# Performance work log

Hardware: AMD Instinct MI355X
Metric: run time of the kernel (lower is better)

The kernel has to match this reference:

```python
import jax, jax.numpy as jnp
import numpy as np


def setup_inputs() -> dict:
    key = jax.random.key(0)
    ks = jax.random.split(key, 7)
    B, Q, K, H, D, R = 2, 2048, 2048, 16, 64, 32
    queries = jax.random.normal(ks[0], (B, Q, H, D), dtype=jnp.float32)
    keys = jax.random.normal(ks[1], (B, K, H, D), dtype=jnp.float32)
    values = jax.random.normal(ks[2], (B, K, H, D), dtype=jnp.float32)
    att_mask = jax.random.randint(ks[3], (B, Q, K), 0, 2, dtype=jnp.int32)
    relative_att_ids = jax.random.randint(ks[4], (B, Q, K), 0, R, dtype=jnp.int32)
    # TruncatedNormal(stddev=0.5) approximated by clipped normal
    relative_emb_table = jnp.clip(
        0.5 * jax.random.normal(ks[5], (R, H, D), dtype=jnp.float32), -1.0, 1.0)
    relative_bias_table = jnp.zeros((R, H), dtype=jnp.float32)
    return {
        'queries': queries,
        'keys': keys,
        'values': values,
        'att_mask': att_mask,
        'relative_att_ids': relative_att_ids,
        'relative_emb_table': relative_emb_table,
        'relative_bias_table': relative_bias_table,
    }


def reference(queries, keys, values, att_mask, relative_att_ids,
              relative_emb_table, relative_bias_table):
    # content scores: [B,Q,K,H]
    content = jnp.einsum('bqhd,bkhd->bqkh', queries, keys)
    # relative scores per vocab id: [B,Q,R,H]
    all_rel = jnp.einsum('bqhd,rhd->bqrh', queries, relative_emb_table)
    all_rel = all_rel + relative_bias_table  # broadcast [R,H]
    # gather along vocab axis per (q,k): [B,Q,K,H]
    rel = jnp.take_along_axis(
        all_rel, relative_att_ids[:, :, :, None].astype(jnp.int32), axis=2)
    scores = content + rel
    d = queries.shape[-1]
    scores = scores / jnp.sqrt(jnp.asarray(d, scores.dtype))
    mask_adder = -10000.0 * (1.0 - att_mask[:, :, :, None].astype(scores.dtype))
    scores = scores + mask_adder
    probs = jax.nn.softmax(scores, axis=-2)  # softmax over key axis
    return jnp.einsum('bqkh,bkhd->bqhd', probs, values)
```

## Files before the change

kernel.cpp:

```cpp
#include <hip/hip_runtime.h>
#include <hip/hip_fp16.h>
#include <stdint.h>

#define Bn 2
#define Qn 2048
#define Kn 2048
#define Hn 16
#define Dn 64
#define Rn 32

#define LOG2E_8 0.18033688011112042f
#define MASK_NEG -14426.950408889634f

typedef __attribute__((ext_vector_type(8))) short short8v;
typedef __attribute__((ext_vector_type(4))) float f32x4;
typedef __attribute__((ext_vector_type(4))) uint32_t u32x4;

static __device__ __forceinline__ uint16_t bf16rn(float f) {
  uint32_t u = __builtin_bit_cast(uint32_t, f);
  u += 0x7FFFu + ((u >> 16) & 1u);
  return (uint16_t)(u >> 16);
}
static __device__ __forceinline__ float bf16f(uint16_t h) {
  uint32_t u = ((uint32_t)h) << 16;
  return __builtin_bit_cast(float, u);
}
static __device__ __forceinline__ float exp2a(float x) {
  float r; asm("v_exp_f32 %0, %1" : "=v"(r) : "v"(x)); return r;
}
static __device__ __forceinline__ uint32_t cvtpk(float lo, float hi) {
  uint32_t r; asm("v_cvt_pk_bf16_f32 %0, %1, %2" : "=v"(r) : "v"(lo), "v"(hi)); return r;
}
static __device__ __forceinline__ void gl_lds16(const void* g, void* l) {
  __builtin_amdgcn_global_load_lds((const __attribute__((address_space(1))) void*)g,
                                   (__attribute__((address_space(3))) void*)l, 16, 0, 0);
}

__global__ void pack_kernel(const int* __restrict__ ids,
                            const int* __restrict__ msk,
                            uint32_t* __restrict__ outp, int n4) {
  int i = blockIdx.x * 256 + threadIdx.x;
  if (i >= n4) return;
  int4 a = reinterpret_cast<const int4*>(ids)[i];
  int4 m = reinterpret_cast<const int4*>(msk)[i];
  uint32_t v = (uint32_t)((a.x | (m.x << 5)) & 0x3f)
             | ((uint32_t)((a.y | (m.y << 5)) & 0x3f) << 8)
             | ((uint32_t)((a.z | (m.z << 5)) & 0x3f) << 16)
             | ((uint32_t)((a.w | (m.w << 5)) & 0x3f) << 24);
  outp[i] = v;
}

__global__ __launch_bounds__(256) void frag_kernel(const float* __restrict__ Kg,
                                                   const float* __restrict__ Vg,
                                                   uint8_t* __restrict__ frag) {
  const int bid = blockIdx.x;
  const int c = bid & 63;
  const int h = (bid >> 6) & 15;
  const int b = bid >> 10;
  uint8_t* panel = frag + (size_t)(b * 16 + h) * 786432u + (size_t)c * 12288u;
  uint4* kf = reinterpret_cast<uint4*>(panel);
  uint4* vf = reinterpret_cast<uint4*>(panel + 8192);
  const int tid = threadIdx.x;
  const int sdq = tid & 7, srow = (tid >> 3) & 15, stile = tid >> 7;
  const int sg = sdq & 3, sdm = sdq >> 2;
  const float* kp = Kg + ((((size_t)b * Kn) + c * 32 + stile * 16 + srow) * Hn + h) * Dn + (sdm * 32 + sg * 4);
  const float4 x0 = *reinterpret_cast<const float4*>(kp);
  const float4 x1 = *reinterpret_cast<const float4*>(kp + 16);
  const float xs0[4] = {x0.x, x0.y, x0.z, x0.w};
  const float xs1[4] = {x1.x, x1.y, x1.z, x1.w};
  uint16_t hh[8], ll[8];
#pragma unroll
  for (int i = 0; i < 4; ++i) {
    const uint16_t h0 = bf16rn(xs0[i]);
    const uint16_t h1 = bf16rn(xs1[i]);
    hh[i] = h0; hh[4 + i] = h1;
    ll[i] = bf16rn(xs0[i] - bf16f(h0));
    ll[4 + i] = bf16rn(xs1[i] - bf16f(h1));
  }
  uint4 uh, ul;
  uh.x = hh[0] | ((uint32_t)hh[1] << 16); uh.y = hh[2] | ((uint32_t)hh[3] << 16);
  uh.z = hh[4] | ((uint32_t)hh[5] << 16); uh.w = hh[6] | ((uint32_t)hh[7] << 16);
  ul.x = ll[0] | ((uint32_t)ll[1] << 16); ul.y = ll[2] | ((uint32_t)ll[3] << 16);
  ul.z = ll[4] | ((uint32_t)ll[5] << 16); ul.w = ll[6] | ((uint32_t)ll[7] << 16);
  kf[(stile * 2 + sdm) * 64 + (srow + 16 * sg)] = uh;
  kf[(4 + stile * 2 + sdm) * 64 + (srow + 16 * sg)] = ul;
  const int vd = tid & 63, vkq = tid >> 6;
  const float* vp = Vg + ((((size_t)b * Kn) + c * 32 + vkq * 4) * Hn + h) * Dn + vd;
  float v0[4], v1[4];
#pragma unroll
  for (int i = 0; i < 4; ++i) {
    v0[i] = vp[i * (Hn * Dn)];
    v1[i] = vp[(16 + i) * (Hn * Dn)];
  }
  uint4 uv;
  uv.x = bf16rn(v0[0]) | ((uint32_t)bf16rn(v0[1]) << 16);
  uv.y = bf16rn(v0[2]) | ((uint32_t)bf16rn(v0[3]) << 16);
  uv.z = bf16rn(v1[0]) | ((uint32_t)bf16rn(v1[1]) << 16);
  uv.w = bf16rn(v1[2]) | ((uint32_t)bf16rn(v1[3]) << 16);
  vf[(vd >> 4) * 64 + (vd & 15) + 16 * vkq] = uv;
}

__global__ __launch_bounds__(256, 2) void attn3_kernel(
    const float* __restrict__ Qg, const float* __restrict__ Eg,
    const float* __restrict__ biasg, const uint8_t* __restrict__ packed,
    const uint8_t* __restrict__ frag, float* __restrict__ outg) {
  __shared__ alignas(16) char smem[66048];
  __half* const tab   = reinterpret_cast<__half*>(smem);
  float* const q_lds  = reinterpret_cast<float*>(smem + 16896);
  float* const et_lds = reinterpret_cast<float*>(smem + 34304);
  char* const cb0 = smem + 16896;
  char* const cb1 = smem + 41472;

  const int tid = threadIdx.x;
  const int lane = tid & 63;
  const int w = tid >> 6;
  const int qr = lane & 15;
  const int g = lane >> 4;

  const int wi = (blockIdx.x & 7) * 64 + (blockIdx.x >> 3);
  const int qt = wi & 15;
  const int h = (wi >> 4) & 15;
  const int b = wi >> 8;
  const int q0 = qt * 128;

  short8v qhi[2][2], qlo[2][2];

#pragma unroll
  for (int half = 0; half < 2; ++half) {
    {
      const int row = tid >> 2, dq = (tid & 3) * 16;
      const float4* s4 = reinterpret_cast<const float4*>(
          Qg + (((size_t)b * Qn + q0 + half * 64 + row) * Hn + h) * Dn + dq);
      float4* dst = reinterpret_cast<float4*>(&q_lds[row * 68 + dq]);
#pragma unroll
      for (int i = 0; i < 4; ++i) dst[i] = s4[i];
    }
    if (half == 0) {
      const int r = tid >> 3, d0 = (tid & 7) * 8;
      const float* src = Eg + ((r * Hn + h) * Dn + d0);
#pragma unroll
      for (int i = 0; i < 8; ++i) et_lds[(d0 + i) * 33 + r] = src[i];
    }
    __syncthreads();
#pragma unroll
    for (int t = 0; t < 2; ++t) {
      const int ql = w * 32 + t * 16 + qr;
      if ((ql >> 6) == half) {
        const int rl = ql & 63;
#pragma unroll
        for (int dm = 0; dm < 2; ++dm) {
#pragma unroll
          for (int j = 0; j < 8; ++j) {
            const int dl = (j < 4) ? (4 * g + j) : (16 + 4 * g + (j - 4));
            const float x = q_lds[rl * 68 + dm * 32 + dl];
            const uint16_t hi = bf16rn(x);
            qhi[t][dm][j] = (short)hi;
            qlo[t][dm][j] = (short)bf16rn(x - bf16f(hi));
          }
        }
      }
    }
    {
      const int r = tid & 31, q8 = tid >> 5;
      float a8[8] = {0.f, 0.f, 0.f, 0.f, 0.f, 0.f, 0.f, 0.f};
      const float bias = biasg[r * Hn + h];
      for (int d = 0; d < 64; ++d) {
        const float e = et_lds[d * 33 + r];
#pragma unroll
        for (int i = 0; i < 8; ++i) a8[i] += e * q_lds[(q8 * 8 + i) * 68 + d];
      }
#pragma unroll
      for (int i = 0; i < 8; ++i) {
        const float ar = LOG2E_8 * (a8[i] + bias);
        const int qq = half * 64 + q8 * 8 + i;
        tab[qq * 66 + r]      = __float2half(ar + MASK_NEG);
        tab[qq * 66 + 32 + r] = __float2half(ar);
      }
    }
    __syncthreads();
  }

  const uint8_t* panel = frag + (size_t)(b * 16 + h) * 786432u;
  const uint8_t* sbase = panel + (size_t)w * 3072 + (size_t)lane * 16;

  const int64_t prow0 = ((int64_t)(b * Qn + q0 + w * 32 + qr)) * Kn + 4 * g;
  const int64_t prow1 = prow0 + (int64_t)16 * Kn;
  const int trow0 = (w * 32 + qr) * 66;
  const int trow1 = trow0 + 16 * 66;

  uint32_t pc[2][4], pn[2][4];
#pragma unroll
  for (int j = 0; j < 4; ++j) {
    pc[0][j] = *(const uint32_t*)(packed + prow0 + j * 16);
    pc[1][j] = *(const uint32_t*)(packed + prow1 + j * 16);
  }

  char* cbc = cb0;
  char* cbn = cb1;
#pragma unroll
  for (int sub = 0; sub < 2; ++sub) {
    const uint8_t* gs = sbase + sub * 12288;
    char* ld = cbc + sub * 12288 + w * 3072;
    gl_lds16(gs, ld); gl_lds16(gs + 1024, ld + 1024); gl_lds16(gs + 2048, ld + 2048);
  }
  asm volatile("s_waitcnt vmcnt(0)" ::: "memory");
  __syncthreads();

  f32x4 acc[2][4] = {{{0.f,0.f,0.f,0.f},{0.f,0.f,0.f,0.f},{0.f,0.f,0.f,0.f},{0.f,0.f,0.f,0.f}},
                     {{0.f,0.f,0.f,0.f},{0.f,0.f,0.f,0.f},{0.f,0.f,0.f,0.f},{0.f,0.f,0.f,0.f}}};
  float mrun[2] = {-1e30f, -1e30f};
  float lrun[2] = {0.f, 0.f};

  for (int c = 0; c < 32; ++c) {
    if (c + 1 < 32) {
#pragma unroll
      for (int sub = 0; sub < 2; ++sub) {
        const uint8_t* gs = sbase + (size_t)(2 * (c + 1) + sub) * 12288u;
        char* ld = cbn + sub * 12288 + w * 3072;
        gl_lds16(gs, ld); gl_lds16(gs + 1024, ld + 1024); gl_lds16(gs + 2048, ld + 2048);
      }
      const int64_t kb = (int64_t)(c + 1) * 64;
#pragma unroll
      for (int j = 0; j < 4; ++j) {
        pn[0][j] = *(const uint32_t*)(packed + prow0 + kb + j * 16);
        pn[1][j] = *(const uint32_t*)(packed + prow1 + kb + j * 16);
      }
    }

    const short8v* kbase = reinterpret_cast<const short8v*>(cbc);
    f32x4 s[2][4] = {{{0.f,0.f,0.f,0.f},{0.f,0.f,0.f,0.f},{0.f,0.f,0.f,0.f},{0.f,0.f,0.f,0.f}},
                     {{0.f,0.f,0.f,0.f},{0.f,0.f,0.f,0.f},{0.f,0.f,0.f,0.f},{0.f,0.f,0.f,0.f}}};
    __builtin_amdgcn_s_setprio(1);
#pragma unroll
    for (int sub = 0; sub < 2; ++sub) {
      const int sb = sub * 768;
#pragma unroll
      for (int dm = 0; dm < 2; ++dm) {
        const short8v k0h = kbase[sb + dm * 64 + lane];
        const short8v k1h = kbase[sb + (2 + dm) * 64 + lane];
        const short8v k0l = kbase[sb + (4 + dm) * 64 + lane];
        const short8v k1l = kbase[sb + (6 + dm) * 64 + lane];
        const int j0 = sub * 2, j1 = sub * 2 + 1;
        s[0][j0] = __builtin_amdgcn_mfma_f32_16x16x32_bf16(k0h, qhi[0][dm], s[0][j0], 0, 0, 0);
        s[0][j0] = __builtin_amdgcn_mfma_f32_16x16x32_bf16(k0l, qhi[0][dm], s[0][j0], 0, 0, 0);
        s[0][j0] = __builtin_amdgcn_mfma_f32_16x16x32_bf16(k0h, qlo[0][dm], s[0][j0], 0, 0, 0);
        s[0][j1] = __builtin_amdgcn_mfma_f32_16x16x32_bf16(k1h, qhi[0][dm], s[0][j1], 0, 0, 0);
        s[0][j1] = __builtin_amdgcn_mfma_f32_16x16x32_bf16(k1l, qhi[0][dm], s[0][j1], 0, 0, 0);
        s[0][j1] = __builtin_amdgcn_mfma_f32_16x16x32_bf16(k1h, qlo[0][dm], s[0][j1], 0, 0, 0);
        s[1][j0] = __builtin_amdgcn_mfma_f32_16x16x32_bf16(k0h, qhi[1][dm], s[1][j0], 0, 0, 0);
        s[1][j0] = __builtin_amdgcn_mfma_f32_16x16x32_bf16(k0l, qhi[1][dm], s[1][j0], 0, 0, 0);
        s[1][j0] = __builtin_amdgcn_mfma_f32_16x16x32_bf16(k0h, qlo[1][dm], s[1][j0], 0, 0, 0);
        s[1][j1] = __builtin_amdgcn_mfma_f32_16x16x32_bf16(k1h, qhi[1][dm], s[1][j1], 0, 0, 0);
        s[1][j1] = __builtin_amdgcn_mfma_f32_16x16x32_bf16(k1l, qhi[1][dm], s[1][j1], 0, 0, 0);
        s[1][j1] = __builtin_amdgcn_mfma_f32_16x16x32_bf16(k1h, qlo[1][dm], s[1][j1], 0, 0, 0);
      }
    }
    __builtin_amdgcn_s_setprio(0);

    short8v vv[2][4];
#pragma unroll
    for (int sub = 0; sub < 2; ++sub) {
      const short8v* vb = reinterpret_cast<const short8v*>(cbc + sub * 12288 + 8192);
#pragma unroll
      for (int dt = 0; dt < 4; ++dt) vv[sub][dt] = vb[dt * 64 + lane];
    }

#pragma unroll
    for (int t = 0; t < 2; ++t) {
      const int trow = t ? trow1 : trow0;
      float sv[16];
#pragma unroll
      for (int i = 0; i < 16; ++i) {
        const int j = i >> 2, r = i & 3;
        const uint32_t v = (pc[t][j] >> (8 * r)) & 63u;
        sv[i] = fmaf(LOG2E_8, s[t][j][r], __half2float(tab[trow + (int)v]));
      }
      float mx = fmaxf(fmaxf(fmaxf(sv[0], sv[1]), fmaxf(sv[2], sv[3])),
                       fmaxf(fmaxf(sv[4], sv[5]), fmaxf(sv[6], sv[7])));
      mx = fmaxf(mx, fmaxf(fmaxf(fmaxf(sv[8], sv[9]), fmaxf(sv[10], sv[11])),
                           fmaxf(fmaxf(sv[12], sv[13]), fmaxf(sv[14], sv[15]))));
      mx = fmaxf(mx, __shfl_xor(mx, 16));
      mx = fmaxf(mx, __shfl_xor(mx, 32));
      if (__any(mx > mrun[t] + 8.f)) {
        const float mnew = fmaxf(mrun[t], mx);
        const float sc = exp2a(mrun[t] - mnew);
        mrun[t] = mnew;
        f32x4 scv;
        scv[0] = __shfl(sc, 4 * g + 0); scv[1] = __shfl(sc, 4 * g + 1);
        scv[2] = __shfl(sc, 4 * g + 2); scv[3] = __shfl(sc, 4 * g + 3);
        acc[t][0] *= scv; acc[t][1] *= scv; acc[t][2] *= scv; acc[t][3] *= scv;
        lrun[t] *= sc;
      }
      float pv[16];
      float ps = 0.f;
#pragma unroll
      for (int i = 0; i < 16; ++i) { pv[i] = exp2a(sv[i] - mrun[t]); ps += pv[i]; }
      lrun[t] += ps;
      u32x4 pu0, pu1;
      pu0[0] = cvtpk(pv[0], pv[1]);  pu0[1] = cvtpk(pv[2], pv[3]);
      pu0[2] = cvtpk(pv[4], pv[5]);  pu0[3] = cvtpk(pv[6], pv[7]);
      pu1[0] = cvtpk(pv[8], pv[9]);  pu1[1] = cvtpk(pv[10], pv[11]);
      pu1[2] = cvtpk(pv[12], pv[13]); pu1[3] = cvtpk(pv[14], pv[15]);
      const short8v pa0 = __builtin_bit_cast(short8v, pu0);
      const short8v pa1 = __builtin_bit_cast(short8v, pu1);
      __builtin_amdgcn_s_setprio(1);
#pragma unroll
      for (int dt = 0; dt < 4; ++dt) {
        acc[t][dt] = __builtin_amdgcn_mfma_f32_16x16x32_bf16(pa0, vv[0][dt], acc[t][dt], 0, 0, 0);
        acc[t][dt] = __builtin_amdgcn_mfma_f32_16x16x32_bf16(pa1, vv[1][dt], acc[t][dt], 0, 0, 0);
      }
      __builtin_amdgcn_s_setprio(0);
    }

#pragma unroll
    for (int j = 0; j < 4; ++j) { pc[0][j] = pn[0][j]; pc[1][j] = pn[1][j]; }

    asm volatile("s_waitcnt vmcnt(0)" ::: "memory");
    __syncthreads();
    char* tmp = cbc; cbc = cbn; cbn = tmp;
  }

#pragma unroll
  for (int t = 0; t < 2; ++t) {
    float lt = lrun[t];
    lt += __shfl_xor(lt, 16);
    lt += __shfl_xor(lt, 32);
    const float linv = 1.0f / lt;
    f32x4 lv;
    lv[0] = __shfl(linv, 4 * g + 0); lv[1] = __shfl(linv, 4 * g + 1);
    lv[2] = __shfl(linv, 4 * g + 2); lv[3] = __shfl(linv, 4 * g + 3);
#pragma unroll
    for (int dt = 0; dt < 4; ++dt) {
#pragma unroll
      for (int r = 0; r < 4; ++r) {
        const int qrow = q0 + w * 32 + t * 16 + 4 * g + r;
        outg[(((size_t)b * Qn + qrow) * Hn + h) * Dn + dt * 16 + qr] = acc[t][dt][r] * lv[r];
      }
    }
  }
}

__global__ __launch_bounds__(256) void attn_old_kernel(
    const float* __restrict__ Qg, const float* __restrict__ Kg,
    const float* __restrict__ Vg, const int* __restrict__ maskg,
    const int* __restrict__ idsg, const float* __restrict__ Eg,
    const float* __restrict__ biasg, float* __restrict__ outg) {
  __shared__ alignas(16) char smem[34304];
  float* const allrel = reinterpret_cast<float*>(smem);
  float* const q_lds  = reinterpret_cast<float*>(smem + 8448);
  float* const et_lds = reinterpret_cast<float*>(smem + 25856);
  uint4* const kfrag  = reinterpret_cast<uint4*>(smem + 8448);
  uint4* const vfrag  = reinterpret_cast<uint4*>(smem + 16640);

  const int tid  = threadIdx.x;
  const int lane = tid & 63;
  const int w    = tid >> 6;
  const int qr   = lane & 15;
  const int g    = lane >> 4;

  const int bid = blockIdx.x;
  const int h  = bid & 15;
  const int qt = (bid >> 4) & 31;
  const int b  = bid >> 9;
  const int q0 = qt * 64;

  {
    const int row = tid >> 2, dq = (tid & 3) * 16;
    const float4* s4 =
        reinterpret_cast<const float4*>(Qg + (((b * Qn) + q0 + row) * Hn + h) * Dn + dq);
    float4* dst = reinterpret_cast<float4*>(&q_lds[row * 68 + dq]);
#pragma unroll
    for (int i = 0; i < 4; ++i) dst[i] = s4[i];
  }
  {
    const int r = tid >> 3, d0 = (tid & 7) * 8;
    const float* src = Eg + ((r * Hn + h) * Dn + d0);
#pragma unroll
    for (int i = 0; i < 8; ++i) et_lds[(d0 + i) * 33 + r] = src[i];
  }
  __syncthreads();

  const int qloc = w * 16 + qr;
  short8v qhi[2], qlo[2];
#pragma unroll
  for (int dm = 0; dm < 2; ++dm) {
#pragma unroll
    for (int j = 0; j < 8; ++j) {
      const int dl = (j < 4) ? (4 * g + j) : (16 + 4 * g + (j - 4));
      const float x = q_lds[qloc * 68 + dm * 32 + dl];
      const uint16_t hi = bf16rn(x);
      qhi[dm][j] = (short)hi;
      qlo[dm][j] = (short)bf16rn(x - bf16f(hi));
    }
  }

  {
    const int r = tid & 31, q8 = tid >> 5;
    float acc[8] = {0.f, 0.f, 0.f, 0.f, 0.f, 0.f, 0.f, 0.f};
    const float bias = biasg[r * Hn + h];
    for (int d = 0; d < 64; ++d) {
      const float e = et_lds[d * 33 + r];
#pragma unroll
      for (int i = 0; i < 8; ++i) acc[i] += e * q_lds[(q8 * 8 + i) * 68 + d];
    }
#pragma unroll
    for (int i = 0; i < 8; ++i)
      allrel[(q8 * 8 + i) * 33 + r] = 0.125f * (acc[i] + bias);
  }
  __syncthreads();

  const int sdq = tid & 7, srow = (tid >> 3) & 15, stile = tid >> 7;
  const int sg = sdq & 3, sdm = sdq >> 2;
  int koff = (((b * Kn) + stile * 16 + srow) * Hn + h) * Dn + (sdm * 32 + sg * 4);
  const int kslotH = (stile * 2 + sdm) * 64 + (srow + 16 * sg);
  const int kslotL = (4 + stile * 2 + sdm) * 64 + (srow + 16 * sg);
  const int vd = tid & 63, vkq = tid >> 6;
  int voff = (((b * Kn) + vkq * 4) * Hn + h) * Dn + vd;
  const int vslot = (vd >> 4) * 64 + (vd & 15) + 16 * vkq;

  const int qglob = q0 + qloc;
  const int prow = (b * Qn + qglob) * Kn + 4 * g;

  f32x4 acc[4] = {{0.f,0.f,0.f,0.f},{0.f,0.f,0.f,0.f},{0.f,0.f,0.f,0.f},{0.f,0.f,0.f,0.f}};
  float mrun = -1e30f, lrun = 0.f;

  const short8v* kfs = reinterpret_cast<const short8v*>(kfrag);
  const short8v* vfs = reinterpret_cast<const short8v*>(vfrag);

  for (int c = 0; c < 64; ++c) {
    const int kb = c * 32;
    __syncthreads();
    {
      const float4 x0 = *reinterpret_cast<const float4*>(Kg + koff);
      const float4 x1 = *reinterpret_cast<const float4*>(Kg + koff + 16);
      koff += 32 * Hn * Dn;
      const float xs0[4] = {x0.x, x0.y, x0.z, x0.w};
      const float xs1[4] = {x1.x, x1.y, x1.z, x1.w};
      uint16_t hh[8], ll[8];
#pragma unroll
      for (int i = 0; i < 4; ++i) {
        const uint16_t h0 = bf16rn(xs0[i]);
        const uint16_t h1 = bf16rn(xs1[i]);
        hh[i] = h0; hh[4 + i] = h1;
        ll[i] = bf16rn(xs0[i] - bf16f(h0));
        ll[4 + i] = bf16rn(xs1[i] - bf16f(h1));
      }
      uint4 uh, ul;
      uh.x = hh[0] | ((uint32_t)hh[1] << 16); uh.y = hh[2] | ((uint32_t)hh[3] << 16);
      uh.z = hh[4] | ((uint32_t)hh[5] << 16); uh.w = hh[6] | ((uint32_t)hh[7] << 16);
      ul.x = ll[0] | ((uint32_t)ll[1] << 16); ul.y = ll[2] | ((uint32_t)ll[3] << 16);
      ul.z = ll[4] | ((uint32_t)ll[5] << 16); ul.w = ll[6] | ((uint32_t)ll[7] << 16);
      kfrag[kslotH] = uh;
      kfrag[kslotL] = ul;
    }
    {
      float v0[4], v1[4];
#pragma unroll
      for (int i = 0; i < 4; ++i) {
        v0[i] = Vg[voff + i * (Hn * Dn)];
        v1[i] = Vg[voff + 16 * Hn * Dn + i * (Hn * Dn)];
      }
      voff += 32 * Hn * Dn;
      uint4 uv;
      uv.x = bf16rn(v0[0]) | ((uint32_t)bf16rn(v0[1]) << 16);
      uv.y = bf16rn(v0[2]) | ((uint32_t)bf16rn(v0[3]) << 16);
      uv.z = bf16rn(v1[0]) | ((uint32_t)bf16rn(v1[1]) << 16);
      uv.w = bf16rn(v1[2]) | ((uint32_t)bf16rn(v1[3]) << 16);
      vfrag[vslot] = uv;
    }
    __syncthreads();

    f32x4 s0 = {0.f, 0.f, 0.f, 0.f}, s1 = {0.f, 0.f, 0.f, 0.f};
#pragma unroll
    for (int dm = 0; dm < 2; ++dm) {
      const short8v k0h = kfs[(dm) * 64 + lane];
      const short8v k1h = kfs[(2 + dm) * 64 + lane];
      const short8v k0l = kfs[(4 + dm) * 64 + lane];
      const short8v k1l = kfs[(6 + dm) * 64 + lane];
      s0 = __builtin_amdgcn_mfma_f32_16x16x32_bf16(k0h, qhi[dm], s0, 0, 0, 0);
      s1 = __builtin_amdgcn_mfma_f32_16x16x32_bf16(k1h, qhi[dm], s1, 0, 0, 0);
      s0 = __builtin_amdgcn_mfma_f32_16x16x32_bf16(k0h, qlo[dm], s0, 0, 0, 0);
      s1 = __builtin_amdgcn_mfma_f32_16x16x32_bf16(k1h, qlo[dm], s1, 0, 0, 0);
      s0 = __builtin_amdgcn_mfma_f32_16x16x32_bf16(k0l, qhi[dm], s0, 0, 0, 0);
      s1 = __builtin_amdgcn_mfma_f32_16x16x32_bf16(k1l, qhi[dm], s1, 0, 0, 0);
    }

    float sv[8];
    {
      const int ib = prow + kb;
      const int4 i0 = *reinterpret_cast<const int4*>(idsg + ib);
      const int4 i1 = *reinterpret_cast<const int4*>(idsg + ib + 16);
      const int4 m0 = *reinterpret_cast<const int4*>(maskg + ib);
      const int4 m1 = *reinterpret_cast<const int4*>(maskg + ib + 16);
      const int ia0[4] = {i0.x, i0.y, i0.z, i0.w};
      const int ia1[4] = {i1.x, i1.y, i1.z, i1.w};
      const int ma0[4] = {m0.x, m0.y, m0.z, m0.w};
      const int ma1[4] = {m1.x, m1.y, m1.z, m1.w};
#pragma unroll
      for (int r = 0; r < 4; ++r) {
        sv[r]     = 0.125f * s0[r] + allrel[qloc * 33 + ia0[r]] + (ma0[r] ? 0.f : -10000.f);
        sv[4 + r] = 0.125f * s1[r] + allrel[qloc * 33 + ia1[r]] + (ma1[r] ? 0.f : -10000.f);
      }
    }

    float m8 = sv[0];
#pragma unroll
    for (int i = 1; i < 8; ++i) m8 = fmaxf(m8, sv[i]);
    m8 = fmaxf(m8, __shfl_xor(m8, 16));
    m8 = fmaxf(m8, __shfl_xor(m8, 32));
    const float mnew = fmaxf(mrun, m8);
    const float sc = __expf(mrun - mnew);
    mrun = mnew;
    float pv[8];
    float ps = 0.f;
#pragma unroll
    for (int i = 0; i < 8; ++i) { pv[i] = __expf(sv[i] - mnew); ps += pv[i]; }
    ps += __shfl_xor(ps, 16);
    ps += __shfl_xor(ps, 32);
    lrun = lrun * sc + ps;

    f32x4 scv;
#pragma unroll
    for (int r = 0; r < 4; ++r) scv[r] = __shfl(sc, 4 * g + r);
#pragma unroll
    for (int dt = 0; dt < 4; ++dt) acc[dt] *= scv;

    short8v pa;
#pragma unroll
    for (int i = 0; i < 8; ++i) pa[i] = (short)bf16rn(pv[i]);
#pragma unroll
    for (int dt = 0; dt < 4; ++dt)
      acc[dt] = __builtin_amdgcn_mfma_f32_16x16x32_bf16(pa, vfs[dt * 64 + lane], acc[dt], 0, 0, 0);
  }

  const float linv = 1.0f / lrun;
  f32x4 lv;
#pragma unroll
  for (int r = 0; r < 4; ++r) lv[r] = __shfl(linv, 4 * g + r);
#pragma unroll
  for (int dt = 0; dt < 4; ++dt) {
#pragma unroll
    for (int r = 0; r < 4; ++r) {
      const int qrow = q0 + w * 16 + 4 * g + r;
      outg[(((b * Qn) + qrow) * Hn + h) * Dn + dt * 16 + qr] = acc[dt][r] * lv[r];
    }
  }
}

extern "C" void kernel_launch(void* const* d_in, const int* in_sizes, int n_in,
                              void* d_out, int out_size, void* d_ws, size_t ws_size,
                              hipStream_t stream) {
  const float* Qg    = (const float*)d_in[0];
  const float* Kg    = (const float*)d_in[1];
  const float* Vg    = (const float*)d_in[2];
  const int*   maskg = (const int*)d_in[3];
  const int*   idsg  = (const int*)d_in[4];
  const float* Eg    = (const float*)d_in[5];
  const float* biasg = (const float*)d_in[6];
  float* outg = (float*)d_out;

  const size_t needPack = (size_t)Bn * Qn * Kn;
  const size_t needFrag = (size_t)Bn * Hn * 64 * 12288;
  const int n4 = (Bn * Qn * Kn) / 4;

  if (ws_size >= needPack + needFrag) {
    pack_kernel<<<n4 / 256, 256, 0, stream>>>(idsg, maskg, (uint32_t*)d_ws, n4);
    frag_kernel<<<Bn * Hn * 64, 256, 0, stream>>>(Kg, Vg, (uint8_t*)d_ws + needPack);
    attn3_kernel<<<Bn * Hn * (Qn / 128), 256, 0, stream>>>(
        Qg, Eg, biasg, (const uint8_t*)d_ws, (const uint8_t*)d_ws + needPack, outg);
  } else {
    attn_old_kernel<<<Bn * Hn * (Qn / 64), 256, 0, stream>>>(
        Qg, Kg, Vg, maskg, idsg, Eg, biasg, outg);
  }
}
```

Baseline: 130.0 us.

## Split key range across two blocks with partial softmax merge kernel

Adds a split-K attention kernel where each block handles half the keys for 128 queries, with smaller LDS and higher occupancy bounds, writing unnormalized accumulators plus running max and sum. A merge kernel then rescales and combines the two partial results into the output. Softmax rescaling is skipped unless the max grows by a threshold. The aim is more blocks in flight and better latency hiding, at the cost of extra global traffic for partials and an additional launch.

```diff
diff --git a/kernel.cpp b/kernel.cpp
--- a/kernel.cpp
+++ b/kernel.cpp
@@ -50,9 +50,9 @@
   outp[i] = v;
 }
 
-__global__ __launch_bounds__(256) void frag_kernel(const float* __restrict__ Kg,
-                                                   const float* __restrict__ Vg,
-                                                   uint8_t* __restrict__ frag) {
+__global__ __launch_bounds__(256) void kfrag_kernel(const float* __restrict__ Kg,
+                                                    const float* __restrict__ Vg,
+                                                    uint8_t* __restrict__ frag) {
   const int bid = blockIdx.x;
   const int c = bid & 63;
   const int h = (bid >> 6) & 15;
@@ -100,6 +100,258 @@
   vf[(vd >> 4) * 64 + (vd & 15) + 16 * vkq] = uv;
 }
 
+__global__ __launch_bounds__(256, 4) void attn5_kernel(
+    const float* __restrict__ Qg, const float* __restrict__ Eg,
+    const float* __restrict__ biasg, const uint8_t* __restrict__ packed,
+    const uint8_t* __restrict__ kfragp, float* __restrict__ acc0p,
+    float* __restrict__ acc1p, float* __restrict__ m0p, float* __restrict__ l0p,
+    float* __restrict__ m1p, float* __restrict__ l1p) {
+  __shared__ alignas(16) char smem[40960];
+  __half* const tab  = reinterpret_cast<__half*>(smem);
+  float* const q_lds = reinterpret_cast<float*>(smem + 16384);
+  float* const et    = reinterpret_cast<float*>(smem + 32768);
+  char* const cb0 = smem + 16384;
+  char* const cb1 = smem + 28672;
+
+  const int tid = threadIdx.x;
+  const int lane = tid & 63;
+  const int w = tid >> 6;
+  const int qr = lane & 15;
+  const int g = lane >> 4;
+
+  const int wi = (blockIdx.x & 7) * 128 + (blockIdx.x >> 3);
+  const int qt = wi & 15;
+  const int ks = (wi >> 4) & 1;
+  const int h = (wi >> 5) & 15;
+  const int b = wi >> 9;
+  const int q0 = qt * 128;
+
+  short8v qhi[2][2], qlo[2][2];
+
+#pragma unroll
+  for (int half = 0; half < 2; ++half) {
+    {
+      const int row = tid >> 2, dq = (tid & 3) * 16;
+      const float4* s4 = reinterpret_cast<const float4*>(
+          Qg + (((size_t)b * Qn + q0 + half * 64 + row) * Hn + h) * Dn + dq);
+      float4* dst = reinterpret_cast<float4*>(&q_lds[row * 64 + dq]);
+#pragma unroll
+      for (int i = 0; i < 4; ++i) dst[i] = s4[i];
+    }
+    if (half == 0) {
+      const int r = tid >> 3, d0 = (tid & 7) * 8;
+      const float* src = Eg + ((r * Hn + h) * Dn + d0);
+#pragma unroll
+      for (int i = 0; i < 8; ++i) et[(d0 + i) * 32 + r] = src[i];
+    }
+    __syncthreads();
+#pragma unroll
+    for (int t = 0; t < 2; ++t) {
+      const int ql = w * 32 + t * 16 + qr;
+      if ((ql >> 6) == half) {
+        const int rl = ql & 63;
+#pragma unroll
+        for (int dm = 0; dm < 2; ++dm) {
+#pragma unroll
+          for (int j = 0; j < 8; ++j) {
+            const int dl = (j < 4) ? (4 * g + j) : (16 + 4 * g + (j - 4));
+            const float x = q_lds[rl * 64 + dm * 32 + dl];
+            const uint16_t hi = bf16rn(x);
+            qhi[t][dm][j] = (short)hi;
+            qlo[t][dm][j] = (short)bf16rn(x - bf16f(hi));
+          }
+        }
+      }
+    }
+    {
+      const int r = tid & 31, q8 = tid >> 5;
+      float a8[8] = {0.f, 0.f, 0.f, 0.f, 0.f, 0.f, 0.f, 0.f};
+      const float bias = biasg[r * Hn + h];
+      for (int d = 0; d < 64; ++d) {
+        const float e = et[d * 32 + r];
+#pragma unroll
+        for (int i = 0; i < 8; ++i) a8[i] += e * q_lds[(q8 * 8 + i) * 64 + d];
+      }
+#pragma unroll
+      for (int i = 0; i < 8; ++i) {
+        const float ar = LOG2E_8 * (a8[i] + bias);
+        const int qq = half * 64 + q8 * 8 + i;
+        tab[qq * 64 + r]      = __float2half(ar + MASK_NEG);
+        tab[qq * 64 + 32 + r] = __float2half(ar);
+      }
+    }
+    __syncthreads();
+  }
+
+  const uint8_t* sbase = kfragp + (size_t)(b * 16 + h) * 786432u +
+                         (size_t)(ks * 32) * 12288u + (size_t)w * 3072 + (size_t)lane * 16;
+  int64_t prow[2];
+  int trow[2];
+#pragma unroll
+  for (int t = 0; t < 2; ++t) {
+    prow[t] = ((int64_t)(b * Qn + q0 + w * 32 + t * 16 + qr)) * Kn + ks * 1024 + 4 * g;
+    trow[t] = (w * 32 + t * 16 + qr) * 64;
+  }
+
+  uint32_t pc[2][2], pn[2][2] = {{0u, 0u}, {0u, 0u}};
+#pragma unroll
+  for (int t = 0; t < 2; ++t)
+#pragma unroll
+    for (int st = 0; st < 2; ++st)
+      pc[t][st] = *reinterpret_cast<const uint32_t*>(packed + prow[t] + st * 16);
+
+  char* cbc = cb0;
+  char* cbn = cb1;
+  {
+    char* ld = cbc + w * 3072;
+    gl_lds16(sbase, ld);
+    gl_lds16(sbase + 1024, ld + 1024);
+    gl_lds16(sbase + 2048, ld + 2048);
+  }
+  asm volatile("s_waitcnt vmcnt(0)" ::: "memory");
+  __syncthreads();
+
+  f32x4 acc[2][4] = {{{0.f,0.f,0.f,0.f},{0.f,0.f,0.f,0.f},{0.f,0.f,0.f,0.f},{0.f,0.f,0.f,0.f}},
+                     {{0.f,0.f,0.f,0.f},{0.f,0.f,0.f,0.f},{0.f,0.f,0.f,0.f},{0.f,0.f,0.f,0.f}}};
+  float mrun[2] = {-1e30f, -1e30f};
+  float lrun[2] = {0.f, 0.f};
+
+  for (int c = 0; c < 32; ++c) {
+    if (c + 1 < 32) {
+      const uint8_t* gs = sbase + (size_t)(c + 1) * 12288u;
+      char* ld = cbn + w * 3072;
+      gl_lds16(gs, ld); gl_lds16(gs + 1024, ld + 1024); gl_lds16(gs + 2048, ld + 2048);
+      const int64_t kb = (int64_t)(c + 1) * 32;
+#pragma unroll
+      for (int t = 0; t < 2; ++t)
+#pragma unroll
+        for (int st = 0; st < 2; ++st)
+          pn[t][st] = *reinterpret_cast<const uint32_t*>(packed + prow[t] + kb + st * 16);
+    }
+
+    const short8v* kfs = reinterpret_cast<const short8v*>(cbc);
+    f32x4 s[2][2] = {{{0.f,0.f,0.f,0.f},{0.f,0.f,0.f,0.f}},
+                     {{0.f,0.f,0.f,0.f},{0.f,0.f,0.f,0.f}}};
+    __builtin_amdgcn_s_setprio(1);
+#pragma unroll
+    for (int dm = 0; dm < 2; ++dm) {
+      const short8v k0h = kfs[dm * 64 + lane];
+      const short8v k1h = kfs[(2 + dm) * 64 + lane];
+      const short8v k0l = kfs[(4 + dm) * 64 + lane];
+      const short8v k1l = kfs[(6 + dm) * 64 + lane];
+#pragma unroll
+      for (int t = 0; t < 2; ++t) {
+        s[t][0] = __builtin_amdgcn_mfma_f32_16x16x32_bf16(k0h, qhi[t][dm], s[t][0], 0, 0, 0);
+        s[t][0] = __builtin_amdgcn_mfma_f32_16x16x32_bf16(k0l, qhi[t][dm], s[t][0], 0, 0, 0);
+        s[t][0] = __builtin_amdgcn_mfma_f32_16x16x32_bf16(k0h, qlo[t][dm], s[t][0], 0, 0, 0);
+        s[t][1] = __builtin_amdgcn_mfma_f32_16x16x32_bf16(k1h, qhi[t][dm], s[t][1], 0, 0, 0);
+        s[t][1] = __builtin_amdgcn_mfma_f32_16x16x32_bf16(k1l, qhi[t][dm], s[t][1], 0, 0, 0);
+        s[t][1] = __builtin_amdgcn_mfma_f32_16x16x32_bf16(k1h, qlo[t][dm], s[t][1], 0, 0, 0);
+      }
+    }
+    __builtin_amdgcn_s_setprio(0);
+
+    const short8v* vfs = reinterpret_cast<const short8v*>(cbc + 8192);
+    short8v vv[4];
+#pragma unroll
+    for (int dt = 0; dt < 4; ++dt) vv[dt] = vfs[dt * 64 + lane];
+
+#pragma unroll
+    for (int t = 0; t < 2; ++t) {
+      float sv[8];
+#pragma unroll
+      for (int st = 0; st < 2; ++st) {
+        const uint32_t pw = pc[t][st];
+#pragma unroll
+        for (int r = 0; r < 4; ++r) {
+          const uint32_t v = (pw >> (8 * r)) & 63u;
+          sv[st * 4 + r] = fmaf(LOG2E_8, s[t][st][r], __half2float(tab[trow[t] + (int)v]));
+        }
+      }
+      float mx = fmaxf(fmaxf(fmaxf(sv[0], sv[1]), fmaxf(sv[2], sv[3])),
+                       fmaxf(fmaxf(sv[4], sv[5]), fmaxf(sv[6], sv[7])));
+      mx = fmaxf(mx, __shfl_xor(mx, 16));
+      mx = fmaxf(mx, __shfl_xor(mx, 32));
+      if (__any(mx > mrun[t] + 8.f)) {
+        const float mnew = fmaxf(mrun[t], mx);
+        const float sc = exp2a(mrun[t] - mnew);
+        mrun[t] = mnew;
+        f32x4 scv;
+        scv[0] = __shfl(sc, 4 * g + 0); scv[1] = __shfl(sc, 4 * g + 1);
+        scv[2] = __shfl(sc, 4 * g + 2); scv[3] = __shfl(sc, 4 * g + 3);
+        acc[t][0] *= scv; acc[t][1] *= scv; acc[t][2] *= scv; acc[t][3] *= scv;
+        lrun[t] *= sc;
+      }
+      float pv[8];
+      float ps = 0.f;
+#pragma unroll
+      for (int i = 0; i < 8; ++i) { pv[i] = exp2a(sv[i] - mrun[t]); ps += pv[i]; }
+      lrun[t] += ps;
+      u32x4 pu;
+      pu[0] = cvtpk(pv[0], pv[1]); pu[1] = cvtpk(pv[2], pv[3]);
+      pu[2] = cvtpk(pv[4], pv[5]); pu[3] = cvtpk(pv[6], pv[7]);
+      const short8v pa = __builtin_bit_cast(short8v, pu);
+      __builtin_amdgcn_s_setprio(1);
+#pragma unroll
+      for (int dt = 0; dt < 4; ++dt)
+        acc[t][dt] = __builtin_amdgcn_mfma_f32_16x16x32_bf16(pa, vv[dt], acc[t][dt], 0, 0, 0);
+      __builtin_amdgcn_s_setprio(0);
+    }
+
+#pragma unroll
+    for (int t = 0; t < 2; ++t) { pc[t][0] = pn[t][0]; pc[t][1] = pn[t][1]; }
+
+    asm volatile("s_waitcnt vmcnt(0)" ::: "memory");
+    __syncthreads();
+    char* tmp = cbc; cbc = cbn; cbn = tmp;
+  }
+
+  float* const accdst = ks ? acc1p : acc0p;
+  float* const mdst = ks ? m1p : m0p;
+  float* const ldst = ks ? l1p : l0p;
+#pragma unroll
+  for (int t = 0; t < 2; ++t) {
+    float lt = lrun[t];
+    lt += __shfl_xor(lt, 16);
+    lt += __shfl_xor(lt, 32);
+    if (lane < 16) {
+      const size_t j = ((size_t)b * Qn + q0 + w * 32 + t * 16 + lane) * Hn + h;
+      mdst[j] = mrun[t];
+      ldst[j] = lt;
+    }
+#pragma unroll
+    for (int dt = 0; dt < 4; ++dt)
+#pragma unroll
+      for (int r = 0; r < 4; ++r) {
+        const int qrow = q0 + w * 32 + t * 16 + 4 * g + r;
+        accdst[(((size_t)b * Qn + qrow) * Hn + h) * Dn + dt * 16 + qr] = acc[t][dt][r];
+      }
+  }
+}
+
+__global__ __launch_bounds__(256) void merge5_kernel(float* __restrict__ out,
+                                                     const float* __restrict__ pp,
+                                                     const float* __restrict__ m0p,
+                                                     const float* __restrict__ l0p,
+                                                     const float* __restrict__ m1p,
+                                                     const float* __restrict__ l1p) {
+  const int i = blockIdx.x * 256 + threadIdx.x;
+  const float4 a = reinterpret_cast<const float4*>(out)[i];
+  const float4 c = reinterpret_cast<const float4*>(pp)[i];
+  const int j = i >> 4;
+  const float m0 = m0p[j], m1 = m1p[j];
+  const float M = fmaxf(m0, m1);
+  const float a0 = exp2a(m0 - M);
+  const float a1 = exp2a(m1 - M);
+  const float inv = 1.0f / (l0p[j] * a0 + l1p[j] * a1);
+  float4 r;
+  r.x = (a.x * a0 + c.x * a1) * inv;
+  r.y = (a.y * a0 + c.y * a1) * inv;
+  r.z = (a.z * a0 + c.z * a1) * inv;
+  r.w = (a.w * a0 + c.w * a1) * inv;
+  reinterpret_cast<float4*>(out)[i] = r;
+}
+
 __global__ __launch_bounds__(256, 2) void attn3_kernel(
     const float* __restrict__ Qg, const float* __restrict__ Eg,
     const float* __restrict__ biasg, const uint8_t* __restrict__ packed,
@@ -185,8 +437,8 @@
 
   const int64_t prow0 = ((int64_t)(b * Qn + q0 + w * 32 + qr)) * Kn + 4 * g;
   const int64_t prow1 = prow0 + (int64_t)16 * Kn;
-  const int trow0 = (w * 32 + qr) * 66;
-  const int trow1 = trow0 + 16 * 66;
+  const int trow0 = (w * 32 + qr);
+  const int trow1 = trow0 + 16;
 
   uint32_t pc[2][4], pn[2][4];
 #pragma unroll
@@ -257,12 +509,12 @@
     }
     __builtin_amdgcn_s_setprio(0);
 
-    short8v vv[2][4];
+    short8v vvx[2][4];
 #pragma unroll
     for (int sub = 0; sub < 2; ++sub) {
       const short8v* vb = reinterpret_cast<const short8v*>(cbc + sub * 12288 + 8192);
 #pragma unroll
-      for (int dt = 0; dt < 4; ++dt) vv[sub][dt] = vb[dt * 64 + lane];
+      for (int dt = 0; dt < 4; ++dt) vvx[sub][dt] = vb[dt * 64 + lane];
     }
 
 #pragma unroll
@@ -272,8 +524,8 @@
 #pragma unroll
       for (int i = 0; i < 16; ++i) {
         const int j = i >> 2, r = i & 3;
-        const uint32_t v = (pc[t][j] >> (8 * r)) & 63u;
-        sv[i] = fmaf(LOG2E_8, s[t][j][r], __half2float(tab[trow + (int)v]));
+        const uint32_t v = ((t ? pc[1][j] : pc[0][j]) >> (8 * r)) & 63u;
+        sv[i] = fmaf(LOG2E_8, t ? s[1][j][r] : s[0][j][r], __half2float(tab[trow * 66 + (int)v]));
       }
       float mx = fmaxf(fmaxf(fmaxf(sv[0], sv[1]), fmaxf(sv[2], sv[3])),
                        fmaxf(fmaxf(sv[4], sv[5]), fmaxf(sv[6], sv[7])));
@@ -306,8 +558,8 @@
       __builtin_amdgcn_s_setprio(1);
 #pragma unroll
       for (int dt = 0; dt < 4; ++dt) {
-        acc[t][dt] = __builtin_amdgcn_mfma_f32_16x16x32_bf16(pa0, vv[0][dt], acc[t][dt], 0, 0, 0);
-        acc[t][dt] = __builtin_amdgcn_mfma_f32_16x16x32_bf16(pa1, vv[1][dt], acc[t][dt], 0, 0, 0);
+        acc[t][dt] = __builtin_amdgcn_mfma_f32_16x16x32_bf16(pa0, vvx[0][dt], acc[t][dt], 0, 0, 0);
+        acc[t][dt] = __builtin_amdgcn_mfma_f32_16x16x32_bf16(pa1, vvx[1][dt], acc[t][dt], 0, 0, 0);
       }
       __builtin_amdgcn_s_setprio(0);
     }
@@ -336,213 +588,6 @@
         const int qrow = q0 + w * 32 + t * 16 + 4 * g + r;
         outg[(((size_t)b * Qn + qrow) * Hn + h) * Dn + dt * 16 + qr] = acc[t][dt][r] * lv[r];
       }
-    }
-  }
-}
-
-__global__ __launch_bounds__(256) void attn_old_kernel(
-    const float* __restrict__ Qg, const float* __restrict__ Kg,
-    const float* __restrict__ Vg, const int* __restrict__ maskg,
-    const int* __restrict__ idsg, const float* __restrict__ Eg,
-    const float* __restrict__ biasg, float* __restrict__ outg) {
-  __shared__ alignas(16) char smem[34304];
-  float* const allrel = reinterpret_cast<float*>(smem);
-  float* const q_lds  = reinterpret_cast<float*>(smem + 8448);
-  float* const et_lds = reinterpret_cast<float*>(smem + 25856);
-  uint4* const kfrag  = reinterpret_cast<uint4*>(smem + 8448);
-  uint4* const vfrag  = reinterpret_cast<uint4*>(smem + 16640);
-
-  const int tid  = threadIdx.x;
-  const int lane = tid & 63;
-  const int w    = tid >> 6;
-  const int qr   = lane & 15;
-  const int g    = lane >> 4;
-
-  const int bid = blockIdx.x;
-  const int h  = bid & 15;
-  const int qt = (bid >> 4) & 31;
-  const int b  = bid >> 9;
-  const int q0 = qt * 64;
-
-  {
-    const int row = tid >> 2, dq = (tid & 3) * 16;
-    const float4* s4 =
-        reinterpret_cast<const float4*>(Qg + (((b * Qn) + q0 + row) * Hn + h) * Dn + dq);
-    float4* dst = reinterpret_cast<float4*>(&q_lds[row * 68 + dq]);
-#pragma unroll
-    for (int i = 0; i < 4; ++i) dst[i] = s4[i];
-  }
-  {
-    const int r = tid >> 3, d0 = (tid & 7) * 8;
-    const float* src = Eg + ((r * Hn + h) * Dn + d0);
-#pragma unroll
-    for (int i = 0; i < 8; ++i) et_lds[(d0 + i) * 33 + r] = src[i];
-  }
-  __syncthreads();
-
-  const int qloc = w * 16 + qr;
-  short8v qhi[2], qlo[2];
-#pragma unroll
-  for (int dm = 0; dm < 2; ++dm) {
-#pragma unroll
-    for (int j = 0; j < 8; ++j) {
-      const int dl = (j < 4) ? (4 * g + j) : (16 + 4 * g + (j - 4));
-      const float x = q_lds[qloc * 68 + dm * 32 + dl];
-      const uint16_t hi = bf16rn(x);
-      qhi[dm][j] = (short)hi;
-      qlo[dm][j] = (short)bf16rn(x - bf16f(hi));
-    }
-  }
-
-  {
-    const int r = tid & 31, q8 = tid >> 5;
-    float acc[8] = {0.f, 0.f, 0.f, 0.f, 0.f, 0.f, 0.f, 0.f};
-    const float bias = biasg[r * Hn + h];
-    for (int d = 0; d < 64; ++d) {
-      const float e = et_lds[d * 33 + r];
-#pragma unroll
-      for (int i = 0; i < 8; ++i) acc[i] += e * q_lds[(q8 * 8 + i) * 68 + d];
-    }
-#pragma unroll
-    for (int i = 0; i < 8; ++i)
-      allrel[(q8 * 8 + i) * 33 + r] = 0.125f * (acc[i] + bias);
-  }
-  __syncthreads();
-
-  const int sdq = tid & 7, srow = (tid >> 3) & 15, stile = tid >> 7;
-  const int sg = sdq & 3, sdm = sdq >> 2;
-  int koff = (((b * Kn) + stile * 16 + srow) * Hn + h) * Dn + (sdm * 32 + sg * 4);
-  const int kslotH = (stile * 2 + sdm) * 64 + (srow + 16 * sg);
-  const int kslotL = (4 + stile * 2 + sdm) * 64 + (srow + 16 * sg);
-  const int vd = tid & 63, vkq = tid >> 6;
-  int voff = (((b * Kn) + vkq * 4) * Hn + h) * Dn + vd;
-  const int vslot = (vd >> 4) * 64 + (vd & 15) + 16 * vkq;
-
-  const int qglob = q0 + qloc;
-  const int prow = (b * Qn + qglob) * Kn + 4 * g;
-
-  f32x4 acc[4] = {{0.f,0.f,0.f,0.f},{0.f,0.f,0.f,0.f},{0.f,0.f,0.f,0.f},{0.f,0.f,0.f,0.f}};
-  float mrun = -1e30f, lrun = 0.f;
-
-  const short8v* kfs = reinterpret_cast<const short8v*>(kfrag);
-  const short8v* vfs = reinterpret_cast<const short8v*>(vfrag);
-
-  for (int c = 0; c < 64; ++c) {
-    const int kb = c * 32;
-    __syncthreads();
-    {
-      const float4 x0 = *reinterpret_cast<const float4*>(Kg + koff);
-      const float4 x1 = *reinterpret_cast<const float4*>(Kg + koff + 16);
-      koff += 32 * Hn * Dn;
-      const float xs0[4] = {x0.x, x0.y, x0.z, x0.w};
-      const float xs1[4] = {x1.x, x1.y, x1.z, x1.w};
-      uint16_t hh[8], ll[8];
-#pragma unroll
-      for (int i = 0; i < 4; ++i) {
-        const uint16_t h0 = bf16rn(xs0[i]);
-        const uint16_t h1 = bf16rn(xs1[i]);
-        hh[i] = h0; hh[4 + i] = h1;
-        ll[i] = bf16rn(xs0[i] - bf16f(h0));
-        ll[4 + i] = bf16rn(xs1[i] - bf16f(h1));
-      }
-      uint4 uh, ul;
-      uh.x = hh[0] | ((uint32_t)hh[1] << 16); uh.y = hh[2] | ((uint32_t)hh[3] << 16);
-      uh.z = hh[4] | ((uint32_t)hh[5] << 16); uh.w = hh[6] | ((uint32_t)hh[7] << 16);
-      ul.x = ll[0] | ((uint32_t)ll[1] << 16); ul.y = ll[2] | ((uint32_t)ll[3] << 16);
-      ul.z = ll[4] | ((uint32_t)ll[5] << 16); ul.w = ll[6] | ((uint32_t)ll[7] << 16);
-      kfrag[kslotH] = uh;
-      kfrag[kslotL] = ul;
-    }
-    {
-      float v0[4], v1[4];
-#pragma unroll
-      for (int i = 0; i < 4; ++i) {
-        v0[i] = Vg[voff + i * (Hn * Dn)];
-        v1[i] = Vg[voff + 16 * Hn * Dn + i * (Hn * Dn)];
-      }
-      voff += 32 * Hn * Dn;
-      uint4 uv;
-      uv.x = bf16rn(v0[0]) | ((uint32_t)bf16rn(v0[1]) << 16);
-      uv.y = bf16rn(v0[2]) | ((uint32_t)bf16rn(v0[3]) << 16);
-      uv.z = bf16rn(v1[0]) | ((uint32_t)bf16rn(v1[1]) << 16);
-      uv.w = bf16rn(v1[2]) | ((uint32_t)bf16rn(v1[3]) << 16);
-      vfrag[vslot] = uv;
-    }
-    __syncthreads();
-
-    f32x4 s0 = {0.f, 0.f, 0.f, 0.f}, s1 = {0.f, 0.f, 0.f, 0.f};
-#pragma unroll
-    for (int dm = 0; dm < 2; ++dm) {
-      const short8v k0h = kfs[(dm) * 64 + lane];
-      const short8v k1h = kfs[(2 + dm) * 64 + lane];
-      const short8v k0l = kfs[(4 + dm) * 64 + lane];
-      const short8v k1l = kfs[(6 + dm) * 64 + lane];
-      s0 = __builtin_amdgcn_mfma_f32_16x16x32_bf16(k0h, qhi[dm], s0, 0, 0, 0);
-      s1 = __builtin_amdgcn_mfma_f32_16x16x32_bf16(k1h, qhi[dm], s1, 0, 0, 0);
-      s0 = __builtin_amdgcn_mfma_f32_16x16x32_bf16(k0h, qlo[dm], s0, 0, 0, 0);
-      s1 = __builtin_amdgcn_mfma_f32_16x16x32_bf16(k1h, qlo[dm], s1, 0, 0, 0);
-      s0 = __builtin_amdgcn_mfma_f32_16x16x32_bf16(k0l, qhi[dm], s0, 0, 0, 0);
-      s1 = __builtin_amdgcn_mfma_f32_16x16x32_bf16(k1l, qhi[dm], s1, 0, 0, 0);
-    }
-
-    float sv[8];
-    {
-      const int ib = prow + kb;
-      const int4 i0 = *reinterpret_cast<const int4*>(idsg + ib);
-      const int4 i1 = *reinterpret_cast<const int4*>(idsg + ib + 16);
-      const int4 m0 = *reinterpret_cast<const int4*>(maskg + ib);
-      const int4 m1 = *reinterpret_cast<const int4*>(maskg + ib + 16);
-      const int ia0[4] = {i0.x, i0.y, i0.z, i0.w};
-      const int ia1[4] = {i1.x, i1.y, i1.z, i1.w};
-      const int ma0[4] = {m0.x, m0.y, m0.z, m0.w};
-      const int ma1[4] = {m1.x, m1.y, m1.z, m1.w};
-#pragma unroll
-      for (int r = 0; r < 4; ++r) {
-        sv[r]     = 0.125f * s0[r] + allrel[qloc * 33 + ia0[r]] + (ma0[r] ? 0.f : -10000.f);
-        sv[4 + r] = 0.125f * s1[r] + allrel[qloc * 33 + ia1[r]] + (ma1[r] ? 0.f : -10000.f);
-      }
-    }
-
-    float m8 = sv[0];
-#pragma unroll
-    for (int i = 1; i < 8; ++i) m8 = fmaxf(m8, sv[i]);
-    m8 = fmaxf(m8, __shfl_xor(m8, 16));
-    m8 = fmaxf(m8, __shfl_xor(m8, 32));
-    const float mnew = fmaxf(mrun, m8);
-    const float sc = __expf(mrun - mnew);
-    mrun = mnew;
-    float pv[8];
-    float ps = 0.f;
-#pragma unroll
-    for (int i = 0; i < 8; ++i) { pv[i] = __expf(sv[i] - mnew); ps += pv[i]; }
-    ps += __shfl_xor(ps, 16);
-    ps += __shfl_xor(ps, 32);
-    lrun = lrun * sc + ps;
-
-    f32x4 scv;
-#pragma unroll
-    for (int r = 0; r < 4; ++r) scv[r] = __shfl(sc, 4 * g + r);
-#pragma unroll
-    for (int dt = 0; dt < 4; ++dt) acc[dt] *= scv;
-
-    short8v pa;
-#pragma unroll
-    for (int i = 0; i < 8; ++i) pa[i] = (short)bf16rn(pv[i]);
-#pragma unroll
-    for (int dt = 0; dt < 4; ++dt)
-      acc[dt] = __builtin_amdgcn_mfma_f32_16x16x32_bf16(pa, vfs[dt * 64 + lane], acc[dt], 0, 0, 0);
-  }
-
-  const float linv = 1.0f / lrun;
-  f32x4 lv;
-#pragma unroll
-  for (int r = 0; r < 4; ++r) lv[r] = __shfl(linv, 4 * g + r);
-#pragma unroll
-  for (int dt = 0; dt < 4; ++dt) {
-#pragma unroll
-    for (int r = 0; r < 4; ++r) {
-      const int qrow = q0 + w * 16 + 4 * g + r;
-      outg[(((b * Qn) + qrow) * Hn + h) * Dn + dt * 16 + qr] = acc[dt][r] * lv[r];
     }
   }
 }
@@ -559,17 +604,33 @@
   const float* biasg = (const float*)d_in[6];
   float* outg = (float*)d_out;
 
-  const size_t needPack = (size_t)Bn * Qn * Kn;
-  const size_t needFrag = (size_t)Bn * Hn * 64 * 12288;
+  const size_t oPack = 0;
+  const size_t oK    = 8388608;
+  const size_t oPP   = 33554432;
+  const size_t oM0   = 50331648;
+  const size_t oL0   = 50593792;
+  const size_t oM1   = 50855936;
+  const size_t oL1   = 51118080;
+  const size_t need5 = 51380224;
+  const size_t need3 = 33554432;
   const int n4 = (Bn * Qn * Kn) / 4;
 
-  if (ws_size >= needPack + needFrag) {
-    pack_kernel<<<n4 / 256, 256, 0, stream>>>(idsg, maskg, (uint32_t*)d_ws, n4);
-    frag_kernel<<<Bn * Hn * 64, 256, 0, stream>>>(Kg, Vg, (uint8_t*)d_ws + needPack);
+  uint8_t* ws = (uint8_t*)d_ws;
+
+  if (ws_size >= need5) {
+    pack_kernel<<<n4 / 256, 256, 0, stream>>>(idsg, maskg, (uint32_t*)(ws + oPack), n4);
+    kfrag_kernel<<<Bn * Hn * 64, 256, 0, stream>>>(Kg, Vg, ws + oK);
+    attn5_kernel<<<Bn * Hn * 2 * (Qn / 128), 256, 0, stream>>>(
+        Qg, Eg, biasg, ws + oPack, ws + oK,
+        outg, (float*)(ws + oPP), (float*)(ws + oM0), (float*)(ws + oL0),
+        (float*)(ws + oM1), (float*)(ws + oL1));
+    merge5_kernel<<<(Bn * Qn * Hn * Dn / 4) / 256, 256, 0, stream>>>(
+        outg, (const float*)(ws + oPP), (const float*)(ws + oM0), (const float*)(ws + oL0),
+        (const float*)(ws + oM1), (const float*)(ws + oL1));
+  } else if (ws_size >= need3) {
+    pack_kernel<<<n4 / 256, 256, 0, stream>>>(idsg, maskg, (uint32_t*)(ws + oPack), n4);
+    kfrag_kernel<<<Bn * Hn * 64, 256, 0, stream>>>(Kg, Vg, ws + oK);
     attn3_kernel<<<Bn * Hn * (Qn / 128), 256, 0, stream>>>(
-        Qg, Eg, biasg, (const uint8_t*)d_ws, (const uint8_t*)d_ws + needPack, outg);
-  } else {
-    attn_old_kernel<<<Bn * Hn * (Qn / 64), 256, 0, stream>>>(
-        Qg, Kg, Vg, maskg, idsg, Eg, biasg, outg);
-  }
-}
+        Qg, Eg, biasg, ws + oPack, ws + oK, outg);
+  }
+}
```

After: 157.2 us. 20.9% more time.
